# Optimization experiments

Measured on AMD Instinct MI355X. Metric: run time of the kernel, lower is better.

## Reference

```python
import jax, jax.numpy as jnp
import numpy as np

# Model constants (match init_kwargs)
H, P, N, G, NL, K = 32, 64, 128, 1, 15, 4   # heads, head_dim, state, groups, lambda levels, conv width
HID, T, BATCH = 1024, 1024, 1
INTER = H * P                    # 2048
CONV_DIM = INTER + 2 * G * N     # 2304
PROJ = INTER + CONV_DIM + H * (NL + 1)  # 4864
EPS = 1e-5


def _level_matrix(t_len: int) -> np.ndarray:
    """Fenwick-tree level assignment: for query t, prefix [0,t] splits into
    power-of-two segments from binary expansion of t+1; segment of length 2^l -> level l."""
    lm = np.zeros((t_len, t_len), dtype=np.int32)
    for t in range(t_len):
        n = t + 1
        while n > 0:
            lb = n & (-n)
            lm[t, n - lb:n] = lb.bit_length() - 1
            n -= lb
    return lm


def setup_inputs() -> dict:
    key = jax.random.key(0)
    ks = jax.random.split(key, 4)
    return {
        "hidden_states": jax.random.normal(ks[0], (BATCH, T, HID), jnp.float32),
        "in_proj_w": jax.random.normal(ks[1], (PROJ, HID), jnp.float32) / np.sqrt(HID).astype(np.float32),
        "in_proj_b": jnp.zeros((PROJ,), jnp.float32),
        "conv_w": jax.random.normal(ks[2], (CONV_DIM, K), jnp.float32) / np.sqrt(K).astype(np.float32),
        "dt_bias": jnp.ones((H,), jnp.float32),
        "A_log": jnp.log(jnp.arange(1, H + 1, dtype=jnp.float32)),
        "L_param": jnp.ones((H, NL), jnp.float32),
        "D": jnp.ones((H,), jnp.float32),
        "rmsnorm_w": jnp.ones((INTER,), jnp.float32),
        "out_proj_w": jax.random.normal(ks[3], (HID, INTER), jnp.float32) / np.sqrt(INTER).astype(np.float32),
        "out_proj_b": jnp.zeros((HID,), jnp.float32),
        "level_mat": jnp.asarray(_level_matrix(T)),  # (T,T) int32, data-independent
    }


def reference(hidden_states, in_proj_w, in_proj_b, conv_w, dt_bias, A_log,
              L_param, D, rmsnorm_w, out_proj_w, out_proj_b, level_mat):
    b, t, _ = hidden_states.shape
    # in_proj and split: [z | xBC | dt | dl]
    zxbcdtdl = hidden_states @ in_proj_w.T + in_proj_b
    z, xBC, dt, dl = jnp.split(zxbcdtdl, [INTER, INTER + CONV_DIM, INTER + CONV_DIM + H], axis=-1)
    # depthwise causal conv1d (width K) + SiLU
    xp = jnp.pad(xBC, ((0, 0), (K - 1, 0), (0, 0)))
    conv = sum(xp[:, w:w + t, :] * conv_w[:, w] for w in range(K))
    xBC = jax.nn.silu(conv)
    x, Bm, Cm = jnp.split(xBC, [INTER, INTER + G * N], axis=-1)
    x = x.reshape(b, t, H, P)          # v pre-scale
    Bm = Bm.reshape(b, t, G, N)        # keys
    Cm = Cm.reshape(b, t, G, N)        # queries
    dl = dl.reshape(b, t, H, NL)
    # D residual uses unscaled x (matches hmamba_chunk_scan_combined ordering)
    D_res = x * D[None, None, :, None]
    dt = jax.nn.softplus(dt + dt_bias)            # (b,t,H)
    v = x * dt[..., None]                          # (b,t,H,P)
    A = -jnp.exp(A_log)                            # (H,)
    g = A * dt                                     # (b,t,H), per-token log-decay (<=0)
    Ls = jax.nn.softplus(L_param * dl)             # (b,t,H,NL) per-token level scales
    # cumulative log-decay; decay(t,s) = exp(cg_t - cg_s), s<=t
    cg = jnp.cumsum(g, axis=1).transpose(0, 2, 1)  # (b,H,t)
    mask = jnp.tril(jnp.ones((t, t), bool))
    logdecay = jnp.where(mask, cg[:, :, :, None] - cg[:, :, None, :], -jnp.inf)
    decay = jnp.exp(logdecay)                      # (b,H,t,s)
    # hierarchical level scale H[t,s] = Ls[b,t,h, level(t,s)]
    Hmat = jnp.take_along_axis(Ls.transpose(0, 2, 1, 3), level_mat[None, None, :, :], axis=-1)  # (b,H,t,s)
    scores = jnp.einsum('btgn,bsgn->bgts', Cm, Bm)  # (b,G,t,s), G=1 broadcasts over heads
    att = scores * decay * Hmat                     # (b,H,t,s), masked via decay=0
    y = jnp.einsum('bhts,bshp->bthp', att, v) + D_res
    y = y.reshape(b, t, INTER)
    # gated RMSNorm with norm_before_gate=False: normalize(y * silu(z)) * w
    yg = y * jax.nn.silu(z)
    y = yg * jax.lax.rsqrt(jnp.mean(yg * yg, axis=-1, keepdims=True) + EPS) * rmsnorm_w
    return y @ out_proj_w.T + out_proj_b
```

## Files before the change

### kernel.cpp

```cpp
#include <hip/hip_runtime.h>
#include <hip/hip_bf16.h>
#include <math.h>

#define T_LEN 1024
#define HID 1024
#define NHEAD 32
#define HDIM 64
#define NSTATE 128
#define NLVL 15
#define KCONV 4
#define INTER 2048
#define CONV_DIM 2304
#define PROJ 4864
#define NPROJ16 4352
#define NPROJF 512
#define EPS 1e-5f

typedef __attribute__((ext_vector_type(8))) _Float16 half8;
typedef __attribute__((ext_vector_type(4))) float float4v;
typedef unsigned short ushort_t;

__device__ __forceinline__ float softplus_f(float x) {
  return fmaxf(x, 0.f) + log1pf(expf(-fabsf(x)));
}
__device__ __forceinline__ float silu_f(float x) {
  return x / (1.f + expf(-x));
}
__device__ __forceinline__ ushort_t f2h(float f) {
  union { _Float16 h; ushort_t u; } v;
  v.h = (_Float16)f;
  return v.u;
}
__device__ __forceinline__ float h2f(ushort_t u) {
  union { ushort_t u; _Float16 h; } v;
  v.u = u;
  return (float)v.h;
}
__device__ __forceinline__ void gload_lds16(const void* g, void* l) {
  __builtin_amdgcn_global_load_lds(
      (const __attribute__((address_space(1))) void*)g,
      (__attribute__((address_space(3))) void*)l, 16, 0, 0);
}

#define N4_HS  (T_LEN * HID / 4)
#define N4_WI  (PROJ * HID / 4)
#define N4_WO  (HID * INTER / 4)
__global__ __launch_bounds__(256) void prep_f16(
    const float* __restrict__ hs, const float* __restrict__ wi,
    const float* __restrict__ wo, ushort_t* __restrict__ hsb,
    ushort_t* __restrict__ wib, ushort_t* __restrict__ wob) {
  int i = blockIdx.x * 256 + threadIdx.x;
  const float* src; ushort_t* dst; int j;
  if (i < N4_HS)              { src = hs; dst = hsb; j = i; }
  else if (i < N4_HS + N4_WI) { src = wi; dst = wib; j = i - N4_HS; }
  else                        { src = wo; dst = wob; j = i - N4_HS - N4_WI; }
  float4 v = reinterpret_cast<const float4*>(src)[j];
  union { ushort_t u[4]; unsigned long long ll; } o;
  o.u[0] = f2h(v.x); o.u[1] = f2h(v.y); o.u[2] = f2h(v.z); o.u[3] = f2h(v.w);
  reinterpret_cast<unsigned long long*>(dst)[j] = o.ll;
}

__global__ __launch_bounds__(256) void gemm_in(
    const ushort_t* __restrict__ A, const ushort_t* __restrict__ B,
    const float* __restrict__ bias,
    ushort_t* __restrict__ Ch, float* __restrict__ Cf) {
  const int K = HID;
  __shared__ ushort_t As[2][128][64];
  __shared__ ushort_t Bs[2][128][64];
  const int tid = threadIdx.x;
  const int w = tid >> 6, L = tid & 63;
  const int n0 = blockIdx.x * 128, m0 = blockIdx.y * 128;
  const int mq = (w & 1) * 64, nq = (w >> 1) * 64;
  const int srow = L >> 3;
  const int swst = ((L & 7) ^ srow) * 8;

  float4v acc[4][4];
#pragma unroll
  for (int i = 0; i < 4; ++i)
#pragma unroll
    for (int j = 0; j < 4; ++j) acc[i][j] = (float4v){0.f, 0.f, 0.f, 0.f};

  const int niter = K / 64;
  {
#pragma unroll
    for (int j = 0; j < 4; ++j) {
      int r0 = 8 * (w * 4 + j);
      gload_lds16(A + (size_t)(m0 + r0 + srow) * K + swst, &As[0][r0][0]);
      gload_lds16(B + (size_t)(n0 + r0 + srow) * K + swst, &Bs[0][r0][0]);
    }
  }
  for (int it = 0; it < niter; ++it) {
    __syncthreads();
    if (it + 1 < niter) {
      const int kk = (it + 1) * 64;
      const int nb = (it + 1) & 1;
#pragma unroll
      for (int j = 0; j < 4; ++j) {
        int r0 = 8 * (w * 4 + j);
        gload_lds16(A + (size_t)(m0 + r0 + srow) * K + kk + swst, &As[nb][r0][0]);
        gload_lds16(B + (size_t)(n0 + r0 + srow) * K + kk + swst, &Bs[nb][r0][0]);
      }
    }
    const int cb = it & 1;
    half8 af[4][2], bf[4][2];
#pragma unroll
    for (int kk2 = 0; kk2 < 2; ++kk2) {
      const int sw = ((kk2 * 4 + (L >> 4)) ^ (L & 7)) * 8;
#pragma unroll
      for (int t = 0; t < 4; ++t) {
        af[t][kk2] = *reinterpret_cast<const half8*>(&As[cb][mq + t * 16 + (L & 15)][sw]);
        bf[t][kk2] = *reinterpret_cast<const half8*>(&Bs[cb][nq + t * 16 + (L & 15)][sw]);
      }
    }
#pragma unroll
    for (int kk2 = 0; kk2 < 2; ++kk2)
#pragma unroll
      for (int mt = 0; mt < 4; ++mt)
#pragma unroll
        for (int nt = 0; nt < 4; ++nt)
          acc[mt][nt] = __builtin_amdgcn_mfma_f32_16x16x32_f16(af[mt][kk2], bf[nt][kk2],
                                                               acc[mt][nt], 0, 0, 0);
  }
  const int qrow = (L >> 4) * 4;
  const bool tof16 = (n0 < NPROJ16);
#pragma unroll
  for (int mt = 0; mt < 4; ++mt) {
#pragma unroll
    for (int nt = 0; nt < 4; ++nt) {
      int col = n0 + nq + nt * 16 + (L & 15);
      float bv = bias[col];
#pragma unroll
      for (int r = 0; r < 4; ++r) {
        int row = m0 + mq + mt * 16 + qrow + r;
        float v = acc[mt][nt][r] + bv;
        if (tof16) Ch[(size_t)row * NPROJ16 + col] = f2h(v);
        else       Cf[(size_t)row * NPROJF + (col - NPROJ16)] = v;
      }
    }
  }
}

__global__ __launch_bounds__(256) void gemm_f16_sk(
    const ushort_t* __restrict__ A, const ushort_t* __restrict__ B,
    float* __restrict__ Cpart, int M, int N, int K, int Kc) {
  __shared__ ushort_t As[2][128][64];
  __shared__ ushort_t Bs[2][128][64];
  const int tid = threadIdx.x;
  const int w = tid >> 6, L = tid & 63;
  const int n0 = blockIdx.x * 128, m0 = blockIdx.y * 128;
  const int kbeg = blockIdx.z * Kc;
  float* __restrict__ C = Cpart + (size_t)blockIdx.z * M * N;
  const int mq = (w & 1) * 64, nq = (w >> 1) * 64;
  const int srow = L >> 3;
  const int swst = ((L & 7) ^ srow) * 8;

  float4v acc[4][4];
#pragma unroll
  for (int i = 0; i < 4; ++i)
#pragma unroll
    for (int j = 0; j < 4; ++j) acc[i][j] = (float4v){0.f, 0.f, 0.f, 0.f};

  const int niter = Kc / 64;
  {
#pragma unroll
    for (int j = 0; j < 4; ++j) {
      int r0 = 8 * (w * 4 + j);
      gload_lds16(A + (size_t)(m0 + r0 + srow) * K + kbeg + swst, &As[0][r0][0]);
      gload_lds16(B + (size_t)(n0 + r0 + srow) * K + kbeg + swst, &Bs[0][r0][0]);
    }
  }
  for (int it = 0; it < niter; ++it) {
    __syncthreads();
    if (it + 1 < niter) {
      const int kk = kbeg + (it + 1) * 64;
      const int nb = (it + 1) & 1;
#pragma unroll
      for (int j = 0; j < 4; ++j) {
        int r0 = 8 * (w * 4 + j);
        gload_lds16(A + (size_t)(m0 + r0 + srow) * K + kk + swst, &As[nb][r0][0]);
        gload_lds16(B + (size_t)(n0 + r0 + srow) * K + kk + swst, &Bs[nb][r0][0]);
      }
    }
    const int cb = it & 1;
    half8 af[4][2], bf[4][2];
#pragma unroll
    for (int kk2 = 0; kk2 < 2; ++kk2) {
      const int sw = ((kk2 * 4 + (L >> 4)) ^ (L & 7)) * 8;
#pragma unroll
      for (int t = 0; t < 4; ++t) {
        af[t][kk2] = *reinterpret_cast<const half8*>(&As[cb][mq + t * 16 + (L & 15)][sw]);
        bf[t][kk2] = *reinterpret_cast<const half8*>(&Bs[cb][nq + t * 16 + (L & 15)][sw]);
      }
    }
#pragma unroll
    for (int kk2 = 0; kk2 < 2; ++kk2)
#pragma unroll
      for (int mt = 0; mt < 4; ++mt)
#pragma unroll
        for (int nt = 0; nt < 4; ++nt)
          acc[mt][nt] = __builtin_amdgcn_mfma_f32_16x16x32_f16(af[mt][kk2], bf[nt][kk2],
                                                               acc[mt][nt], 0, 0, 0);
  }
  const int qrow = (L >> 4) * 4;
#pragma unroll
  for (int mt = 0; mt < 4; ++mt) {
#pragma unroll
    for (int nt = 0; nt < 4; ++nt) {
      int col = n0 + nq + nt * 16 + (L & 15);
#pragma unroll
      for (int r = 0; r < 4; ++r) {
        int row = m0 + mq + mt * 16 + qrow + r;
        C[(size_t)row * N + col] = acc[mt][nt][r];
      }
    }
  }
}

__global__ __launch_bounds__(256) void reduce_out4(const float* __restrict__ p,
                                                   const float* __restrict__ bias,
                                                   float* __restrict__ out, int MN) {
  int i = blockIdx.x * 256 + threadIdx.x;
  if (i * 4 >= MN) return;
  float4 a = reinterpret_cast<const float4*>(p)[i];
  float4 b = reinterpret_cast<const float4*>(p + MN)[i];
  float4 c = reinterpret_cast<const float4*>(p + 2 * (size_t)MN)[i];
  float4 d = reinterpret_cast<const float4*>(p + 3 * (size_t)MN)[i];
  int col = (i * 4) & (HID - 1);
  float4 bv = *reinterpret_cast<const float4*>(bias + col);
  float4 o;
  o.x = a.x + b.x + c.x + d.x + bv.x;
  o.y = a.y + b.y + c.y + d.y + bv.y;
  o.z = a.z + b.z + c.z + d.z + bv.z;
  o.w = a.w + b.w + c.w + d.w + bv.w;
  reinterpret_cast<float4*>(out)[i] = o;
}

__global__ __launch_bounds__(512) void pointwise_dt(
    const float* __restrict__ zxf, const float* __restrict__ dt_bias,
    const float* __restrict__ A_log, const float* __restrict__ L_param,
    float* __restrict__ dtbuf, float* __restrict__ gT,
    float* __restrict__ Lsbuf) {
  const int t = blockIdx.x;
  const int j = threadIdx.x;
  const size_t ro = (size_t)t * NPROJF;
  if (j < NHEAD * NLVL) {
    float x = L_param[j] * zxf[ro + NHEAD + j];
    Lsbuf[(size_t)t * (NHEAD * NLVL) + j] = softplus_f(x);
  } else {
    int h = j - NHEAD * NLVL;
    float x = zxf[ro + h] + dt_bias[h];
    float dt = softplus_f(x);
    dtbuf[t * NHEAD + h] = dt;
    gT[h * T_LEN + t] = -expf(A_log[h]) * dt;
  }
}

__global__ __launch_bounds__(64) void scan_g(const float* __restrict__ gT,
                                             double* __restrict__ cgd) {
  const int h = blockIdx.x, l = threadIdx.x;
  const float* gr = gT + (size_t)h * T_LEN + l * 16;
  double pre[16];
  double acc = 0.0;
#pragma unroll
  for (int i = 0; i < 16; ++i) { acc += (double)gr[i]; pre[i] = acc; }
  double s = acc;
#pragma unroll
  for (int off = 1; off < 64; off <<= 1) {
    double o = __shfl_up(s, off, 64);
    if (l >= off) s += o;
  }
  const double base = s - acc;
  double* cr = cgd + (size_t)h * T_LEN + l * 16;
#pragma unroll
  for (int i = 0; i < 16; ++i) cr[i] = base + pre[i];
}

__global__ __launch_bounds__(256) void conv_fused(
    const ushort_t* __restrict__ zxh, const float* __restrict__ conv_w,
    const float* __restrict__ dtbuf, const float* __restrict__ Dp,
    ushort_t* __restrict__ vt, float* __restrict__ ybuf,
    ushort_t* __restrict__ Bb, ushort_t* __restrict__ Cb) {
  __shared__ ushort_t Vl[64][68];
  __shared__ float dtl[64];
  const int tq = blockIdx.x, cy = blockIdx.y;
  const int t0 = tq * 64;
  const int tid = threadIdx.x;
  const int lane = tid & 63, g = tid >> 6;
  const bool vpath = (cy < 32);
  const int ccol = vpath ? cy * 64 + lane : INTER + (cy - 32) * 64 + lane;
  const int zcol = INTER + ccol;
  float cw[KCONV];
#pragma unroll
  for (int w = 0; w < KCONV; ++w) cw[w] = conv_w[ccol * KCONV + w];
  if (vpath && tid < 64) dtl[tid] = dtbuf[(t0 + tid) * NHEAD + cy];
  const float Dh = vpath ? Dp[cy] : 0.f;

  float xv[19];
#pragma unroll
  for (int i = 0; i < 19; ++i) {
    int tt = t0 + g * 16 - 3 + i;
    if (tt >= 0) {
      xv[i] = h2f(zxh[(size_t)tt * NPROJ16 + zcol]);
    } else xv[i] = 0.f;
  }
  __syncthreads();
#pragma unroll
  for (int i = 0; i < 16; ++i) {
    float acc = xv[i] * cw[0] + xv[i + 1] * cw[1] + xv[i + 2] * cw[2] + xv[i + 3] * cw[3];
    float sil = silu_f(acc);
    int tl = g * 16 + i;
    int t = t0 + tl;
    if (vpath) {
      ushort_t vh = f2h(sil * dtl[tl]);
      Vl[tl][lane] = vh;
      ybuf[(size_t)t * INTER + cy * 64 + lane] = sil * Dh;
    } else if (ccol < INTER + NSTATE) {
      Bb[t * NSTATE + (ccol - INTER)] = f2h(sil);
    } else {
      Cb[t * NSTATE + (ccol - INTER - NSTATE)] = f2h(sil);
    }
  }
  if (vpath) {
    __syncthreads();
#pragma unroll
    for (int rep = 0; rep < 2; ++rep) {
      int u = tid + 256 * rep;
      int p = u >> 3, t8 = (u & 7) * 8;
      union { ushort_t u16[8]; half8 h; } o;
#pragma unroll
      for (int j = 0; j < 8; ++j) o.u16[j] = Vl[t8 + j][p];
      *reinterpret_cast<half8*>(vt + (size_t)(cy * 64 + p) * T_LEN + t0 + t8) = o.h;
    }
  }
}

__global__ __launch_bounds__(256) void qk_gemm(
    const ushort_t* __restrict__ Cq, const ushort_t* __restrict__ Bk,
    ushort_t* __restrict__ S) {
  const int idx = blockIdx.x;
  int qt = (int)(0.5f * (sqrtf(8.f * (float)idx + 1.f) - 1.f));
  if ((qt + 1) * (qt + 2) / 2 <= idx) ++qt;
  if (qt * (qt + 1) / 2 > idx) --qt;
  const int st = idx - qt * (qt + 1) / 2;
  const int tid = threadIdx.x, w = tid >> 6, L = tid & 63;
  const int q0 = qt * 64 + (w & 1) * 32;
  const int s0 = st * 64 + (w >> 1) * 32;

  half8 af[2][4], bf[2][4];
#pragma unroll
  for (int mt = 0; mt < 2; ++mt)
#pragma unroll
    for (int ks = 0; ks < 4; ++ks) {
      af[mt][ks] = *reinterpret_cast<const half8*>(
          Cq + (size_t)(q0 + mt * 16 + (L & 15)) * NSTATE + ks * 32 + (L >> 4) * 8);
      bf[mt][ks] = *reinterpret_cast<const half8*>(
          Bk + (size_t)(s0 + mt * 16 + (L & 15)) * NSTATE + ks * 32 + (L >> 4) * 8);
    }
  float4v acc[2][2];
#pragma unroll
  for (int i = 0; i < 2; ++i)
#pragma unroll
    for (int j = 0; j < 2; ++j) acc[i][j] = (float4v){0.f, 0.f, 0.f, 0.f};
#pragma unroll
  for (int ks = 0; ks < 4; ++ks)
#pragma unroll
    for (int mt = 0; mt < 2; ++mt)
#pragma unroll
      for (int nt = 0; nt < 2; ++nt)
        acc[mt][nt] = __builtin_amdgcn_mfma_f32_16x16x32_f16(af[mt][ks], bf[nt][ks],
                                                             acc[mt][nt], 0, 0, 0);
  const int qrow = (L >> 4) * 4;
#pragma unroll
  for (int mt = 0; mt < 2; ++mt)
#pragma unroll
    for (int nt = 0; nt < 2; ++nt) {
      int col = s0 + nt * 16 + (L & 15);
#pragma unroll
      for (int r = 0; r < 4; ++r)
        S[(size_t)(q0 + mt * 16 + qrow + r) * T_LEN + col] = f2h(acc[mt][nt][r]);
    }
}

__global__ __launch_bounds__(256) void attn_mfma(
    const ushort_t* __restrict__ S, const ushort_t* __restrict__ vt,
    const double* __restrict__ cgd, const float* __restrict__ Lsb,
    float* __restrict__ ybuf) {
  __shared__ ushort_t Vtl[64][72];
  __shared__ float Lsl[64][17];
  __shared__ __align__(16) float cgq[64];
  __shared__ __align__(16) float cgs[64];

  const int item = blockIdx.x;
  const int h = item & 31;
  const int qt = 15 - (item >> 5);

  const int tid = threadIdx.x;
  const int w = tid >> 6, L = tid & 63;
  const int tq0 = qt * 64;
  const double* cgh = cgd + (size_t)h * T_LEN;
  const double base = cgh[tq0];

  for (int i = tid; i < 64 * NLVL; i += 256) {
    int r = i / NLVL, l = i - r * NLVL;
    Lsl[r][l] = Lsb[(size_t)(tq0 + r) * (NHEAD * NLVL) + h * NLVL + l];
  }
  if (tid < 64) cgq[tid] = (float)(cgh[tq0 + tid] - base);

  float4v yac[4];
#pragma unroll
  for (int i = 0; i < 4; ++i) yac[i] = (float4v){0.f, 0.f, 0.f, 0.f};

  const int qloc = w * 16 + (L & 15);
  const int tg = tq0 + qloc;
  const int qrow = w * 16 + ((L >> 4) << 2);

  for (int st = 0; st <= qt; ++st) {
    const int ts0 = st * 64;
    __syncthreads();
    half8 sv0 = *reinterpret_cast<const half8*>(
        S + (size_t)tg * T_LEN + ts0 + (L >> 4) * 8);
    half8 sv1 = *reinterpret_cast<const half8*>(
        S + (size_t)tg * T_LEN + ts0 + 32 + (L >> 4) * 8);
#pragma unroll
    for (int i = 0; i < 2; ++i) {
      int u = tid + 256 * i;
      int p = u >> 3, sc = (u & 7) * 8;
      *reinterpret_cast<half8*>(&Vtl[p][sc]) =
          *reinterpret_cast<const half8*>(vt + (size_t)(h * HDIM + p) * T_LEN + ts0 + sc);
    }
    if (tid < 64) cgs[tid] = (float)(cgh[ts0 + tid] - base);
    __syncthreads();

    const float cq = cgq[qloc];
    half8 af[2];
#pragma unroll
    for (int ks = 0; ks < 2; ++ks) {
      const half8 sv = ks ? sv1 : sv0;
      const int sb = ks * 32 + (L >> 4) * 8;
      float4 c0 = *reinterpret_cast<const float4*>(&cgs[sb]);
      float4 c1 = *reinterpret_cast<const float4*>(&cgs[sb + 4]);
      float csv[8] = {c0.x, c0.y, c0.z, c0.w, c1.x, c1.y, c1.z, c1.w};
      union { ushort_t u[8]; half8 h; } o;
#pragma unroll
      for (int jj = 0; jj < 8; ++jj) {
        int sg = ts0 + sb + jj;
        float val = 0.f;
        if (sg <= tg) {
          int lvl = 31 - __clz((unsigned)(sg ^ (tg + 1)));
          val = (float)sv[jj] * __expf(cq - csv[jj]) * Lsl[qloc][lvl];
        }
        o.u[jj] = f2h(val);
      }
      af[ks] = o.h;
    }
#pragma unroll
    for (int ks = 0; ks < 2; ++ks) {
#pragma unroll
      for (int pt = 0; pt < 4; ++pt) {
        half8 bfv = *reinterpret_cast<const half8*>(&Vtl[pt * 16 + (L & 15)][ks * 32 + (L >> 4) * 8]);
        yac[pt] = __builtin_amdgcn_mfma_f32_16x16x32_f16(af[ks], bfv, yac[pt], 0, 0, 0);
      }
    }
  }
#pragma unroll
  for (int pt = 0; pt < 4; ++pt) {
    int p = pt * 16 + (L & 15);
#pragma unroll
    for (int r = 0; r < 4; ++r) {
      int q = qrow + r;
      float* dst = ybuf + (size_t)(tq0 + q) * INTER + h * HDIM + p;
      *dst += yac[pt][r];
    }
  }
}

__global__ __launch_bounds__(256) void rmsnorm_gate(
    const float* __restrict__ ybuf, const ushort_t* __restrict__ zxh,
    const float* __restrict__ w, ushort_t* __restrict__ yhf) {
  __shared__ float red[4];
  const int t = blockIdx.x, tid = threadIdx.x;
  const size_t ro = (size_t)t * NPROJ16;
  const float* yrow = ybuf + (size_t)t * INTER;
  float yg[8];
  float ss = 0.f;
#pragma unroll
  for (int i = 0; i < 8; ++i) {
    int c = tid + 256 * i;
    float z = h2f(zxh[ro + c]);
    float g = yrow[c] * silu_f(z);
    yg[i] = g;
    ss += g * g;
  }
#pragma unroll
  for (int off = 32; off; off >>= 1) ss += __shfl_down(ss, off, 64);
  if ((tid & 63) == 0) red[tid >> 6] = ss;
  __syncthreads();
  if (tid == 0) red[0] = red[0] + red[1] + red[2] + red[3];
  __syncthreads();
  const float scale = rsqrtf(red[0] / (float)INTER + EPS);
#pragma unroll
  for (int i = 0; i < 8; ++i) {
    int c = tid + 256 * i;
    yhf[(size_t)t * INTER + c] = f2h(yg[i] * scale * w[c]);
  }
}

extern "C" void kernel_launch(void* const* d_in, const int* in_sizes, int n_in,
                              void* d_out, int out_size, void* d_ws, size_t ws_size,
                              hipStream_t stream) {
  const float* hs        = (const float*)d_in[0];
  const float* in_proj_w = (const float*)d_in[1];
  const float* in_proj_b = (const float*)d_in[2];
  const float* conv_w    = (const float*)d_in[3];
  const float* dt_bias   = (const float*)d_in[4];
  const float* A_log     = (const float*)d_in[5];
  const float* L_param   = (const float*)d_in[6];
  const float* Dp        = (const float*)d_in[7];
  const float* rms_w     = (const float*)d_in[8];
  const float* out_proj_w= (const float*)d_in[9];
  const float* out_proj_b= (const float*)d_in[10];
  float* out = (float*)d_out;

  char* W = (char*)d_ws;
  size_t off = 0;
  auto alloc = [&](size_t bytes) { void* p = W + off; off = (off + bytes + 255) & ~(size_t)255; return p; };
  double*   cgd = (double*)  alloc((size_t)NHEAD * T_LEN * 8);
  float*    zxf = (float*)   alloc((size_t)T_LEN * NPROJF * 4);
  float*    opp = (float*)   alloc((size_t)4 * T_LEN * HID * 4);
  float*    ybuf= (float*)   alloc((size_t)T_LEN * INTER * 4);
  float*    gT  = (float*)   alloc((size_t)NHEAD * T_LEN * 4);
  float*    dtb = (float*)   alloc((size_t)T_LEN * NHEAD * 4);
  float*    Lsb = (float*)   alloc((size_t)T_LEN * NHEAD * NLVL * 4);
  ushort_t* zxh = (ushort_t*)alloc((size_t)T_LEN * NPROJ16 * 2);
  ushort_t* hsb = (ushort_t*)alloc((size_t)T_LEN * HID * 2);
  ushort_t* Wib = (ushort_t*)alloc((size_t)PROJ * HID * 2);
  ushort_t* Wob = (ushort_t*)alloc((size_t)HID * INTER * 2);
  ushort_t* yhf = (ushort_t*)alloc((size_t)T_LEN * INTER * 2);
  ushort_t* vt  = (ushort_t*)alloc((size_t)T_LEN * INTER * 2);
  ushort_t* Bb  = (ushort_t*)alloc((size_t)T_LEN * NSTATE * 2);
  ushort_t* Cb  = (ushort_t*)alloc((size_t)T_LEN * NSTATE * 2);
  ushort_t* Sbuf= (ushort_t*)alloc((size_t)T_LEN * T_LEN * 2);

  prep_f16<<<(N4_HS + N4_WI + N4_WO) / 256, 256, 0, stream>>>(
      hs, in_proj_w, out_proj_w, hsb, Wib, Wob);

  gemm_in<<<dim3(PROJ / 128, T_LEN / 128), 256, 0, stream>>>(
      hsb, Wib, in_proj_b, zxh, zxf);

  pointwise_dt<<<T_LEN, 512, 0, stream>>>(zxf, dt_bias, A_log, L_param, dtb, gT, Lsb);

  scan_g<<<NHEAD, 64, 0, stream>>>(gT, cgd);

  conv_fused<<<dim3(T_LEN / 64, 36), 256, 0, stream>>>(
      zxh, conv_w, dtb, Dp, vt, ybuf, Bb, Cb);

  qk_gemm<<<136, 256, 0, stream>>>(Cb, Bb, Sbuf);

  attn_mfma<<<NHEAD * 16, 256, 0, stream>>>(Sbuf, vt, cgd, Lsb, ybuf);

  rmsnorm_gate<<<T_LEN, 256, 0, stream>>>(ybuf, zxh, rms_w, yhf);

  gemm_f16_sk<<<dim3(HID / 128, T_LEN / 128, 4), 256, 0, stream>>>(
      yhf, Wob, opp, T_LEN, HID, INTER, INTER / 4);
  reduce_out4<<<(T_LEN * HID / 4 + 255) / 256, 256, 0, stream>>>(
      opp, out_proj_b, out, T_LEN * HID);
}
```

Baseline: 207.5 us.

## Split causal attention key range across blocks with atomic accumulation

Each (head, query-tile) work item is split into chunks of up to two key tiles, giving 72 blocks per head instead of 16. This balances the triangular causal workload and raises occupancy. Partial outputs are combined with float atomicAdd into ybuf, which adds atomic traffic and makes the summation order nondeterministic. The causal-mask check is also skipped for off-diagonal tiles, where every entry is already valid.

```diff
diff --git a/kernel.cpp b/kernel.cpp
--- a/kernel.cpp
+++ b/kernel.cpp
@@ -391,8 +391,14 @@
   __shared__ __align__(16) float cgs[64];
 
   const int item = blockIdx.x;
-  const int h = item & 31;
-  const int qt = 15 - (item >> 5);
+  const int h = item / 72;
+  int rem = item - h * 72;
+  int qt = 0, j = 0;
+  for (int q = 0; q < 16; ++q) {
+    int cnt = (q + 2) >> 1;
+    if (rem < cnt) { qt = q; j = rem; break; }
+    rem -= cnt;
+  }
 
   const int tid = threadIdx.x;
   const int w = tid >> 6, L = tid & 63;
@@ -414,7 +420,9 @@
   const int tg = tq0 + qloc;
   const int qrow = w * 16 + ((L >> 4) << 2);
 
-  for (int st = 0; st <= qt; ++st) {
+  const int st0 = 2 * j;
+  const int st1 = min(2 * j + 2, qt + 1);
+  for (int st = st0; st < st1; ++st) {
     const int ts0 = st * 64;
     __syncthreads();
     half8 sv0 = *reinterpret_cast<const half8*>(
@@ -433,25 +441,44 @@
 
     const float cq = cgq[qloc];
     half8 af[2];
-#pragma unroll
-    for (int ks = 0; ks < 2; ++ks) {
-      const half8 sv = ks ? sv1 : sv0;
-      const int sb = ks * 32 + (L >> 4) * 8;
-      float4 c0 = *reinterpret_cast<const float4*>(&cgs[sb]);
-      float4 c1 = *reinterpret_cast<const float4*>(&cgs[sb + 4]);
-      float csv[8] = {c0.x, c0.y, c0.z, c0.w, c1.x, c1.y, c1.z, c1.w};
-      union { ushort_t u[8]; half8 h; } o;
-#pragma unroll
-      for (int jj = 0; jj < 8; ++jj) {
-        int sg = ts0 + sb + jj;
-        float val = 0.f;
-        if (sg <= tg) {
+    if (st < qt) {
+#pragma unroll
+      for (int ks = 0; ks < 2; ++ks) {
+        const half8 sv = ks ? sv1 : sv0;
+        const int sb = ks * 32 + (L >> 4) * 8;
+        float4 c0 = *reinterpret_cast<const float4*>(&cgs[sb]);
+        float4 c1 = *reinterpret_cast<const float4*>(&cgs[sb + 4]);
+        float csv[8] = {c0.x, c0.y, c0.z, c0.w, c1.x, c1.y, c1.z, c1.w};
+        union { ushort_t u[8]; half8 h; } o;
+#pragma unroll
+        for (int jj = 0; jj < 8; ++jj) {
+          int sg = ts0 + sb + jj;
           int lvl = 31 - __clz((unsigned)(sg ^ (tg + 1)));
-          val = (float)sv[jj] * __expf(cq - csv[jj]) * Lsl[qloc][lvl];
+          o.u[jj] = f2h((float)sv[jj] * __expf(cq - csv[jj]) * Lsl[qloc][lvl]);
         }
-        o.u[jj] = f2h(val);
-      }
-      af[ks] = o.h;
+        af[ks] = o.h;
+      }
+    } else {
+#pragma unroll
+      for (int ks = 0; ks < 2; ++ks) {
+        const half8 sv = ks ? sv1 : sv0;
+        const int sb = ks * 32 + (L >> 4) * 8;
+        float4 c0 = *reinterpret_cast<const float4*>(&cgs[sb]);
+        float4 c1 = *reinterpret_cast<const float4*>(&cgs[sb + 4]);
+        float csv[8] = {c0.x, c0.y, c0.z, c0.w, c1.x, c1.y, c1.z, c1.w};
+        union { ushort_t u[8]; half8 h; } o;
+#pragma unroll
+        for (int jj = 0; jj < 8; ++jj) {
+          int sg = ts0 + sb + jj;
+          float val = 0.f;
+          if (sg <= tg) {
+            int lvl = 31 - __clz((unsigned)(sg ^ (tg + 1)));
+            val = (float)sv[jj] * __expf(cq - csv[jj]) * Lsl[qloc][lvl];
+          }
+          o.u[jj] = f2h(val);
+        }
+        af[ks] = o.h;
+      }
     }
 #pragma unroll
     for (int ks = 0; ks < 2; ++ks) {
@@ -468,8 +495,7 @@
 #pragma unroll
     for (int r = 0; r < 4; ++r) {
       int q = qrow + r;
-      float* dst = ybuf + (size_t)(tq0 + q) * INTER + h * HDIM + p;
-      *dst += yac[pt][r];
+      atomicAdd(ybuf + (size_t)(tq0 + q) * INTER + h * HDIM + p, yac[pt][r]);
     }
   }
 }
@@ -556,7 +582,7 @@
 
   qk_gemm<<<136, 256, 0, stream>>>(Cb, Bb, Sbuf);
 
-  attn_mfma<<<NHEAD * 16, 256, 0, stream>>>(Sbuf, vt, cgd, Lsb, ybuf);
+  attn_mfma<<<NHEAD * 72, 256, 0, stream>>>(Sbuf, vt, cgd, Lsb, ybuf);
 
   rmsnorm_gate<<<T_LEN, 256, 0, stream>>>(ybuf, zxh, rms_w, yhf);
 
```

Result: no change. 205.3 us (-1.1%).
